# Kernel optimization log

Measured on AMD Instinct MI355X. Metric: run time of the kernel, lower is better.

The kernel has to match this reference:

```python
import jax, jax.numpy as jnp
import numpy as np

K_UNF = 11   # unfold kernel = 15 - 4
PAD = 1      # reflection padding for attention branch
KC = 5       # ConvBlock kernel_conv
HEADS = 4
CIN = 64
HD = CIN // HEADS  # head_dim = 16
EPS = 1e-5


def _unfold(x, k):
    # x: [b,C,H,W] -> [b, C*k*k, oh*ow] with torch.nn.Unfold ordering (c, kh, kw)
    b, C, H, W = x.shape
    oh, ow = H - k + 1, W - k + 1
    ih = jnp.arange(oh)[:, None] + jnp.arange(k)[None, :]  # [oh,k]
    iw = jnp.arange(ow)[:, None] + jnp.arange(k)[None, :]  # [ow,k]
    p = x[:, :, ih, :]          # [b,C,oh,k,W]
    p = p[:, :, :, :, iw]       # [b,C,oh,k,ow,k]
    p = p.transpose(0, 1, 3, 5, 2, 4)  # [b,C,kh,kw,oh,ow]
    return p.reshape(b, C * k * k, oh * ow)


def _bn_train(x):
    # BatchNorm2d in training mode, weight=1, bias=0 (fresh module defaults)
    m = x.mean(axis=(0, 2, 3), keepdims=True)
    v = x.var(axis=(0, 2, 3), keepdims=True)
    return (x - m) * jax.lax.rsqrt(v + EPS)


def setup_inputs() -> dict:
    key = jax.random.key(0)
    ks = jax.random.split(key, 6)
    b = 64
    s = 0.02
    x1 = jax.random.normal(ks[0], (b, CIN, 15, 15), jnp.float32)
    Wq = jax.random.normal(ks[1], (CIN, CIN), jnp.float32) * s
    Wk = jax.random.normal(ks[2], (CIN, CIN), jnp.float32) * s
    Wv = jax.random.normal(ks[3], (CIN, CIN), jnp.float32) * s
    fc_w = jax.random.normal(ks[4], (KC * KC, 3 * HEADS), jnp.float32) * s
    convg_w = jax.random.normal(ks[5], (CIN, CIN, 3, 3), jnp.float32) * s
    # dep_conv weight: deterministic one-hot shift kernels per reset_parameters
    dk = np.zeros((KC * KC, KC, KC), np.float32)
    for i in range(KC * KC):
        dk[i, i // KC, i % KC] = 1.0
    dep_w = jnp.asarray(np.broadcast_to(dk[None], (CIN, KC * KC, KC, KC)).copy())
    return {"x1": x1, "Wq": Wq, "Wk": Wk, "Wv": Wv, "fc_w": fc_w,
            "dep_w": dep_w, "convg_w": convg_w}


def reference(x1, Wq, Wk, Wv, fc_w, dep_w, convg_w):
    b, C, h, w = x1.shape  # h=w=15 (i=1 -> size=15)
    size = h
    # 1x1 qkv convs
    q = jnp.einsum('oc,bchw->bohw', Wq, x1)
    k = jnp.einsum('oc,bchw->bohw', Wk, x1)
    v = jnp.einsum('oc,bchw->bohw', Wv, x1)
    # ---- conv branch (ConvBlock) ----
    qkv = jnp.concatenate([t.reshape(b, HEADS, HD, h * w) for t in (q, k, v)], axis=1)  # [b,12,16,225]
    f_all = jnp.einsum('oc,bcds->bods', fc_w, qkv)                 # [b,25,16,225]
    f_conv = f_all.transpose(0, 2, 1, 3).reshape(b, HD * KC * KC, h, w)  # [b,400,15,15]
    out_conv = jax.lax.conv_general_dilated(
        f_conv, dep_w, (1, 1), 'VALID',
        dimension_numbers=('NCHW', 'OIHW', 'NCHW'),
        feature_group_count=HD)                                     # [b,64,11,11]; bias is None
    out_conv = _bn_train(out_conv)
    # ---- attention branch (UnfoldBlock + raw scaled QK^T, no softmax) ----
    def pad_unfold(t):
        tp = jnp.pad(t, ((0, 0), (0, 0), (PAD, PAD), (PAD, PAD)), mode='reflect')
        u = _unfold(tp, K_UNF).transpose(0, 2, 1)  # [b,49,7744]; pos_embed is zeros
        cls = jnp.zeros((b, 1, u.shape[-1]), u.dtype)  # cls token params are zeros
        return jnp.concatenate([cls, u], axis=1)       # [b,50,7744]
    uq, uk, uv = pad_unfold(q), pad_unfold(k), pad_unfold(v)
    N, Cq = uq.shape[1], uq.shape[2]
    query = uq.reshape(b, HEADS, N, Cq // HEADS)  # matches torch reshape semantics
    key_ = uk.reshape(b, HEADS, N, Cq // HEADS)
    val = uv.reshape(b, HEADS, N, Cq // HEADS)
    scaling = float(HD) ** -0.5
    att = jnp.einsum('bhnc,bhmc->bhnm', query, key_) * scaling   # [b,4,50,50]
    out_attn = jnp.einsum('bhnm,bhmc->bhnc', att, val)
    out_attn = out_attn.transpose(0, 2, 1, 3).reshape(b, N, Cq)
    out_attn = out_attn[:, 1, :].reshape(b, CIN, size - 4, size - 4)  # [b,64,11,11]
    out_attn = jax.lax.conv_general_dilated(
        out_attn, convg_w, (1, 1), ((1, 1), (1, 1)),
        dimension_numbers=('NCHW', 'OIHW', 'NCHW'))
    # rate1 and rate2 are filled with 0.5 every forward
    return out_conv * 0.5 + out_attn * 0.5
```

## Files before the change

kernel.cpp:

```cpp
#include <hip/hip_runtime.h>
#include <hip/hip_bf16.h>

#define B 64
#define CIN 64
#define HW 225
#define CQ 7744

__device__ __forceinline__ int reflect15(int t) {
    return t < 0 ? -t : (t > 14 ? 28 - t : t);
}
__device__ __forceinline__ int refp(int t) { return reflect15(t - 1); }

__global__ void qkv_kernel(const float* __restrict__ x1,
                           const float* __restrict__ Wq,
                           const float* __restrict__ Wk,
                           const float* __restrict__ Wv,
                           float* __restrict__ q, float* __restrict__ k, float* __restrict__ v) {
    int b = blockIdx.x;
    int t = blockIdx.y;
    const float* W = (t == 0) ? Wq : (t == 1) ? Wk : Wv;
    float* out = (t == 0) ? q : (t == 1) ? k : v;
    __shared__ float xs[CIN * HW];
    __shared__ float wsm[CIN * CIN];
    const float* xb = x1 + (size_t)b * CIN * HW;
    for (int i = threadIdx.x; i < CIN * HW; i += 512) xs[i] = xb[i];
    for (int i = threadIdx.x; i < CIN * CIN; i += 512) wsm[i] = W[i];
    __syncthreads();
    int og = threadIdx.x >> 5;
    int ls = threadIdx.x & 31;
    float a0[8] = {0,0,0,0,0,0,0,0};
    float a1[8] = {0,0,0,0,0,0,0,0};
    float a2[8] = {0,0,0,0,0,0,0,0};
    float a3[8] = {0,0,0,0,0,0,0,0};
    for (int c = 0; c < CIN; ++c) {
        const float* xc = xs + c * HW;
        float xv[8];
        #pragma unroll
        for (int j = 0; j < 8; ++j) {
            int s = ls + 32 * j;
            xv[j] = (s < HW) ? xc[s] : 0.f;
        }
        float w0 = wsm[(og)      * CIN + c];
        float w1 = wsm[(og + 16) * CIN + c];
        float w2 = wsm[(og + 32) * CIN + c];
        float w3 = wsm[(og + 48) * CIN + c];
        #pragma unroll
        for (int j = 0; j < 8; ++j) {
            a0[j] += w0 * xv[j];
            a1[j] += w1 * xv[j];
            a2[j] += w2 * xv[j];
            a3[j] += w3 * xv[j];
        }
    }
    float* ob = out + (size_t)b * CIN * HW;
    #pragma unroll
    for (int j = 0; j < 8; ++j) {
        int s = ls + 32 * j;
        if (s < HW) {
            ob[(og)      * HW + s] = a0[j];
            ob[(og + 16) * HW + s] = a1[j];
            ob[(og + 32) * HW + s] = a2[j];
            ob[(og + 48) * HW + s] = a3[j];
        }
    }
}

__global__ void conv5_kernel(const float* __restrict__ q, const float* __restrict__ k,
                             const float* __restrict__ v, const float* __restrict__ fc_w,
                             float* __restrict__ ocpre, float* __restrict__ stats) {
    int b = blockIdx.x, g = blockIdx.y;
    __shared__ float chs[12][HW];
    __shared__ float fw[300];
    __shared__ float red[128], red2[128];
    const float* srcs[3] = {q, k, v};
    for (int i = threadIdx.x; i < 12 * HW; i += blockDim.x) {
        int c = i / HW, s = i % HW;
        int t = c >> 2, hd = c & 3;
        chs[c][s] = srcs[t][(size_t)b * CIN * HW + (hd * 16 + g) * HW + s];
    }
    for (int i = threadIdx.x; i < 300; i += blockDim.x) fw[i] = fc_w[i];
    __syncthreads();
    float myval = 0.f;
    int yx = threadIdx.x;
    if (yx < 121) {
        int y = yx / 11, x = yx % 11;
        float acc = 0.f;
        #pragma unroll
        for (int c = 0; c < 12; ++c) {
            #pragma unroll
            for (int kh = 0; kh < 5; ++kh) {
                #pragma unroll
                for (int kw = 0; kw < 5; ++kw) {
                    acc += fw[(kh * 5 + kw) * 12 + c] * chs[c][(y + kh) * 15 + (x + kw)];
                }
            }
        }
        ocpre[((size_t)b * 16 + g) * 121 + yx] = acc;
        myval = acc;
    }
    red[threadIdx.x] = myval;
    red2[threadIdx.x] = myval * myval;
    __syncthreads();
    for (int s = 64; s > 0; s >>= 1) {
        if (threadIdx.x < s) {
            red[threadIdx.x] += red[threadIdx.x + s];
            red2[threadIdx.x] += red2[threadIdx.x + s];
        }
        __syncthreads();
    }
    if (threadIdx.x == 0) {
        atomicAdd(&stats[g], red[0]);
        atomicAdd(&stats[16 + g], red2[0]);
    }
}

__global__ void qk_kernel(const float* __restrict__ q, const float* __restrict__ k,
                          float* __restrict__ att_g) {
    int b = blockIdx.x, hh = blockIdx.y, qq = blockIdx.z;
    __shared__ float kp[16 * 289];
    __shared__ float qw[16 * 121];
    int tid = threadIdx.x;
    const float* kb = k + ((size_t)b * CIN + qq * 16) * HW;
    for (int i = tid; i < 16 * 289; i += 256) {
        int ch = i / 289, rr = i % 289;
        int yy = rr / 17, xx = rr % 17;
        kp[i] = kb[ch * HW + refp(yy) * 15 + refp(xx)];
    }
    {
        int gq = 50 * hh + 1;
        int rq = gq >> 2;
        if (rq == 0) {
            for (int i = tid; i < 16 * 121; i += 256) qw[i] = 0.f;
        } else {
            int cq = (gq & 3) * 16;
            int p = rq - 1, py0 = p / 7, px0 = p % 7;
            const float* qb = q + ((size_t)b * CIN + cq) * HW;
            for (int i = tid; i < 16 * 121; i += 256) {
                int cl = i / 121, rr = i % 121;
                int ki = rr / 11, kj = rr % 11;
                qw[i] = qb[cl * HW + refp(py0 + ki) * 15 + refp(px0 + kj)];
            }
        }
    }
    __syncthreads();
    int wave = tid >> 6, lane = tid & 63;
    int m0 = (qq - 2 * hh) & 3;
    int nt = (50 - m0 + 3) >> 2;
    float* ag = att_g + ((size_t)b * 4 + hh) * 64;
    for (int t = wave; t < nt; t += 4) {
        int m = m0 + t * 4;
        int g = 50 * hh + m;
        int r = g >> 2;
        float acc = 0.f;
        if (r > 0) {
            int p = r - 1, py = p / 7, px = p % 7;
            #pragma unroll
            for (int it = 0; it < 3; ++it) {
                int rw = lane + it * 64;
                if (rw < 176) {
                    int cl = rw / 11, ki = rw % 11;
                    const float* kr = kp + cl * 289 + (py + ki) * 17 + px;
                    const float* qr = qw + cl * 121 + ki * 11;
                    float s = 0.f;
                    #pragma unroll
                    for (int kj = 0; kj < 11; ++kj) s += qr[kj] * kr[kj];
                    acc += s;
                }
            }
            #pragma unroll
            for (int off = 32; off > 0; off >>= 1) acc += __shfl_xor(acc, off);
        }
        if (lane == 0) ag[m] = acc * 0.25f;
    }
}

__global__ void pv_kernel(const float* __restrict__ v, const float* __restrict__ att_g,
                          float* __restrict__ attn_img) {
    int b = blockIdx.x, hh = blockIdx.y, clg = blockIdx.z;
    __shared__ float vp[16 * 289];
    __shared__ float attmap[4 * 49];
    int tid = threadIdx.x;
    const float* vb = v + (size_t)b * CIN * HW;
    for (int i = tid; i < 16 * 289; i += 256) {
        int idx = i / 289, rr = i % 289;
        int qq2 = idx >> 2, cs = idx & 3;
        int yy = rr / 17, xx = rr % 17;
        vp[i] = vb[(qq2 * 16 + clg * 4 + cs) * HW + refp(yy) * 15 + refp(xx)];
    }
    if (tid < 4 * 49) attmap[tid] = 0.f;
    __syncthreads();
    if (tid < 50) {
        int g = 50 * hh + tid;
        int r = g >> 2;
        if (r > 0) attmap[(g & 3) * 49 + (r - 1)] = att_g[((size_t)b * 4 + hh) * 64 + tid];
    }
    __syncthreads();
    float* outp = attn_img + (size_t)b * CQ + hh * 1936 + clg * 4 * 121;
    if (tid < 242) {
        #pragma unroll
        for (int half = 0; half < 2; ++half) {
            int o = tid + half * 242;
            int cs = o / 121, yx = o % 121;
            int y = yx / 11, x = yx % 11;
            float acc = 0.f;
            #pragma unroll
            for (int qq2 = 0; qq2 < 4; ++qq2) {
                const float* vc = vp + (qq2 * 4 + cs) * 289 + y * 17 + x;
                const float* am = attmap + qq2 * 49;
                #pragma unroll
                for (int py = 0; py < 7; ++py) {
                    #pragma unroll
                    for (int px = 0; px < 7; ++px) {
                        acc += am[py * 7 + px] * vc[py * 17 + px];
                    }
                }
            }
            outp[cs * 121 + yx] = acc;
        }
    }
}

__global__ __launch_bounds__(512, 2) void final_kernel(
                             const float* __restrict__ ocpre, const float* __restrict__ stats,
                             const float* __restrict__ attn_img, const float* __restrict__ convg_w,
                             float* __restrict__ out) {
    int b = blockIdx.x, og = blockIdx.y;
    __shared__ float ap[CIN * 169];
    __shared__ float wsm[8 * CIN * 12];
    __shared__ float red[3 * 8 * 128];
    int tid = threadIdx.x;
    for (int i = tid; i < CIN * 169; i += 512) ap[i] = 0.f;
    for (int i = tid; i < 8 * CIN * 9; i += 512) {
        int oc = i / 9, t = i % 9;
        wsm[oc * 12 + t] = convg_w[(size_t)og * 8 * CIN * 9 + i];
    }
    __syncthreads();
    for (int i = tid; i < CIN * 121; i += 512) {
        int c = i / 121, ss = i % 121;
        ap[c * 169 + (ss / 11 + 1) * 13 + (ss % 11 + 1)] = attn_img[(size_t)b * CQ + i];
    }
    __syncthreads();
    int quarter = tid >> 7;
    int slot = tid & 127;
    int px = slot < 121 ? slot : 120;
    int y = px / 11, x = px % 11;
    float f0 = 0.f, f1 = 0.f, f2 = 0.f, f3 = 0.f, f4 = 0.f, f5 = 0.f, f6 = 0.f, f7 = 0.f;
    #pragma unroll 2
    for (int c16 = 0; c16 < 16; ++c16) {
        int c = quarter * 16 + c16;
        const float* apc = ap + c * 169 + y * 13 + x;
        float a00 = apc[0],  a01 = apc[1],  a02 = apc[2];
        float a10 = apc[13], a11 = apc[14], a12 = apc[15];
        float a20 = apc[26], a21 = apc[27], a22 = apc[28];
        const float4* wq = (const float4*)wsm;
        #pragma unroll
        for (int oo = 0; oo < 8; ++oo) {
            float4 wA = wq[(oo * 64 + c) * 3 + 0];
            float4 wB = wq[(oo * 64 + c) * 3 + 1];
            float4 wC = wq[(oo * 64 + c) * 3 + 2];
            float s = wA.x * a00 + wA.y * a01 + wA.z * a02
                    + wA.w * a10 + wB.x * a11 + wB.y * a12
                    + wB.z * a20 + wB.w * a21 + wC.x * a22;
            switch (oo) {
                case 0: f0 += s; break; case 1: f1 += s; break;
                case 2: f2 += s; break; case 3: f3 += s; break;
                case 4: f4 += s; break; case 5: f5 += s; break;
                case 6: f6 += s; break; case 7: f7 += s; break;
            }
        }
    }
    if (quarter > 0) {
        float* r = red + (quarter - 1) * 1024 + slot;
        r[0 * 128] = f0; r[1 * 128] = f1; r[2 * 128] = f2; r[3 * 128] = f3;
        r[4 * 128] = f4; r[5 * 128] = f5; r[6 * 128] = f6; r[7 * 128] = f7;
    }
    __syncthreads();
    if (quarter == 0 && slot < 121) {
        #pragma unroll
        for (int qq = 0; qq < 3; ++qq) {
            const float* r = red + qq * 1024 + slot;
            f0 += r[0 * 128]; f1 += r[1 * 128]; f2 += r[2 * 128]; f3 += r[3 * 128];
            f4 += r[4 * 128]; f5 += r[5 * 128]; f6 += r[6 * 128]; f7 += r[7 * 128];
        }
        int g0 = og * 2, g1 = og * 2 + 1;
        float m0 = stats[g0] * (1.f / 7744.f);
        float m1 = stats[g1] * (1.f / 7744.f);
        float v0 = stats[16 + g0] * (1.f / 7744.f) - m0 * m0;
        float v1 = stats[16 + g1] * (1.f / 7744.f) - m1 * m1;
        float r0 = rsqrtf(v0 + 1e-5f);
        float r1 = rsqrtf(v1 + 1e-5f);
        float bn0 = (ocpre[((size_t)b * 16 + g0) * 121 + slot] - m0) * r0;
        float bn1 = (ocpre[((size_t)b * 16 + g1) * 121 + slot] - m1) * r1;
        float* ob = out + ((size_t)b * CIN + og * 8) * 121 + slot;
        ob[0 * 121] = 0.5f * bn0 + 0.5f * f0;
        ob[1 * 121] = 0.5f * bn0 + 0.5f * f1;
        ob[2 * 121] = 0.5f * bn0 + 0.5f * f2;
        ob[3 * 121] = 0.5f * bn0 + 0.5f * f3;
        ob[4 * 121] = 0.5f * bn1 + 0.5f * f4;
        ob[5 * 121] = 0.5f * bn1 + 0.5f * f5;
        ob[6 * 121] = 0.5f * bn1 + 0.5f * f6;
        ob[7 * 121] = 0.5f * bn1 + 0.5f * f7;
    }
}

extern "C" void kernel_launch(void* const* d_in, const int* in_sizes, int n_in,
                              void* d_out, int out_size, void* d_ws, size_t ws_size,
                              hipStream_t stream) {
    const float* x1     = (const float*)d_in[0];
    const float* Wq     = (const float*)d_in[1];
    const float* Wk     = (const float*)d_in[2];
    const float* Wv     = (const float*)d_in[3];
    const float* fc_w   = (const float*)d_in[4];
    const float* convg_w = (const float*)d_in[6];
    float* out = (float*)d_out;

    char* ws = (char*)d_ws;
    float* q        = (float*)(ws);
    float* k        = (float*)(ws + 3686400);
    float* v        = (float*)(ws + 7372800);
    float* ocpre    = (float*)(ws + 11059200);
    float* stats    = (float*)(ws + 11554816);
    float* attn_img = (float*)(ws + 11555072);
    float* att_g    = (float*)(ws + 13537536);

    hipMemsetAsync(stats, 0, 32 * sizeof(float), stream);
    hipLaunchKernelGGL(qkv_kernel, dim3(64, 3), dim3(512), 0, stream, x1, Wq, Wk, Wv, q, k, v);
    hipLaunchKernelGGL(conv5_kernel, dim3(64, 16), dim3(128), 0, stream, q, k, v, fc_w, ocpre, stats);
    hipLaunchKernelGGL(qk_kernel, dim3(64, 4, 4), dim3(256), 0, stream, q, k, att_g);
    hipLaunchKernelGGL(pv_kernel, dim3(64, 4, 4), dim3(256), 0, stream, v, att_g, attn_img);
    hipLaunchKernelGGL(final_kernel, dim3(64, 8), dim3(512), 0, stream, ocpre, stats, attn_img, convg_w, out);
}
```

Measured before the change: 167.6 us.

## Register-tile qkv, restructure pv, fold memset, read weights directly from global

The qkv kernel now uses 256 threads, each computing an 8x8 register tile from padded shared x and a transposed weight copy with float4 loads. It also zeroes the stats buffer itself, which removes the separate memset. pv_kernel merges the channel-group grid dimension so one block loads all 64 padded v channels, and it broadcasts attention weights with readlane while each thread computes six output pixels. conv5 and final now read fc_w and convg_w straight from global memory instead of staging them in shared memory. The stats zeroing depends on kernel ordering on the same stream, and the direct global weight reads may cost more if they are not turned into scalar loads.

```diff
diff --git a/kernel.cpp b/kernel.cpp
--- a/kernel.cpp
+++ b/kernel.cpp
@@ -5,62 +5,62 @@
 #define CIN 64
 #define HW 225
 #define CQ 7744
+#define XSP 232
 
 __device__ __forceinline__ int reflect15(int t) {
     return t < 0 ? -t : (t > 14 ? 28 - t : t);
 }
 __device__ __forceinline__ int refp(int t) { return reflect15(t - 1); }
 
-__global__ void qkv_kernel(const float* __restrict__ x1,
+__global__ __launch_bounds__(256) void qkv_kernel(const float* __restrict__ x1,
                            const float* __restrict__ Wq,
                            const float* __restrict__ Wk,
                            const float* __restrict__ Wv,
-                           float* __restrict__ q, float* __restrict__ k, float* __restrict__ v) {
+                           float* __restrict__ q, float* __restrict__ k, float* __restrict__ v,
+                           float* __restrict__ stats) {
     int b = blockIdx.x;
     int t = blockIdx.y;
+    if (b == 0 && t == 0 && threadIdx.x < 32) stats[threadIdx.x] = 0.f;
     const float* W = (t == 0) ? Wq : (t == 1) ? Wk : Wv;
     float* out = (t == 0) ? q : (t == 1) ? k : v;
-    __shared__ float xs[CIN * HW];
-    __shared__ float wsm[CIN * CIN];
+    __shared__ float xs[CIN * XSP];
+    __shared__ float wsmT[CIN * CIN];
     const float* xb = x1 + (size_t)b * CIN * HW;
-    for (int i = threadIdx.x; i < CIN * HW; i += 512) xs[i] = xb[i];
-    for (int i = threadIdx.x; i < CIN * CIN; i += 512) wsm[i] = W[i];
+    for (int i = threadIdx.x; i < CIN * XSP; i += 256) {
+        int c = i / XSP, s = i % XSP;
+        xs[i] = (s < HW) ? xb[c * HW + s] : 0.f;
+    }
+    for (int i = threadIdx.x; i < CIN * CIN; i += 256) {
+        wsmT[i] = W[(i & 63) * CIN + (i >> 6)];
+    }
     __syncthreads();
     int og = threadIdx.x >> 5;
     int ls = threadIdx.x & 31;
-    float a0[8] = {0,0,0,0,0,0,0,0};
-    float a1[8] = {0,0,0,0,0,0,0,0};
-    float a2[8] = {0,0,0,0,0,0,0,0};
-    float a3[8] = {0,0,0,0,0,0,0,0};
+    float acc[8][8];
+    #pragma unroll
+    for (int m = 0; m < 8; ++m)
+        #pragma unroll
+        for (int j = 0; j < 8; ++j) acc[m][j] = 0.f;
     for (int c = 0; c < CIN; ++c) {
-        const float* xc = xs + c * HW;
-        float xv[8];
-        #pragma unroll
-        for (int j = 0; j < 8; ++j) {
-            int s = ls + 32 * j;
-            xv[j] = (s < HW) ? xc[s] : 0.f;
-        }
-        float w0 = wsm[(og)      * CIN + c];
-        float w1 = wsm[(og + 16) * CIN + c];
-        float w2 = wsm[(og + 32) * CIN + c];
-        float w3 = wsm[(og + 48) * CIN + c];
-        #pragma unroll
-        for (int j = 0; j < 8; ++j) {
-            a0[j] += w0 * xv[j];
-            a1[j] += w1 * xv[j];
-            a2[j] += w2 * xv[j];
-            a3[j] += w3 * xv[j];
-        }
+        float4 xv0 = *(const float4*)(xs + c * XSP + ls * 8);
+        float4 xv1 = *(const float4*)(xs + c * XSP + ls * 8 + 4);
+        float4 wv0 = *(const float4*)(wsmT + c * CIN + og * 8);
+        float4 wv1 = *(const float4*)(wsmT + c * CIN + og * 8 + 4);
+        float xr[8] = {xv0.x, xv0.y, xv0.z, xv0.w, xv1.x, xv1.y, xv1.z, xv1.w};
+        float wr[8] = {wv0.x, wv0.y, wv0.z, wv0.w, wv1.x, wv1.y, wv1.z, wv1.w};
+        #pragma unroll
+        for (int m = 0; m < 8; ++m)
+            #pragma unroll
+            for (int j = 0; j < 8; ++j) acc[m][j] += wr[m] * xr[j];
     }
     float* ob = out + (size_t)b * CIN * HW;
     #pragma unroll
-    for (int j = 0; j < 8; ++j) {
-        int s = ls + 32 * j;
-        if (s < HW) {
-            ob[(og)      * HW + s] = a0[j];
-            ob[(og + 16) * HW + s] = a1[j];
-            ob[(og + 32) * HW + s] = a2[j];
-            ob[(og + 48) * HW + s] = a3[j];
+    for (int m = 0; m < 8; ++m) {
+        int o = og * 8 + m;
+        #pragma unroll
+        for (int j = 0; j < 8; ++j) {
+            int px = ls * 8 + j;
+            if (px < HW) ob[o * HW + px] = acc[m][j];
         }
     }
 }
@@ -70,7 +70,6 @@
                              float* __restrict__ ocpre, float* __restrict__ stats) {
     int b = blockIdx.x, g = blockIdx.y;
     __shared__ float chs[12][HW];
-    __shared__ float fw[300];
     __shared__ float red[128], red2[128];
     const float* srcs[3] = {q, k, v};
     for (int i = threadIdx.x; i < 12 * HW; i += blockDim.x) {
@@ -78,7 +77,6 @@
         int t = c >> 2, hd = c & 3;
         chs[c][s] = srcs[t][(size_t)b * CIN * HW + (hd * 16 + g) * HW + s];
     }
-    for (int i = threadIdx.x; i < 300; i += blockDim.x) fw[i] = fc_w[i];
     __syncthreads();
     float myval = 0.f;
     int yx = threadIdx.x;
@@ -91,7 +89,7 @@
             for (int kh = 0; kh < 5; ++kh) {
                 #pragma unroll
                 for (int kw = 0; kw < 5; ++kw) {
-                    acc += fw[(kh * 5 + kw) * 12 + c] * chs[c][(y + kh) * 15 + (x + kw)];
+                    acc += fc_w[(kh * 5 + kw) * 12 + c] * chs[c][(y + kh) * 15 + (x + kw)];
                 }
             }
         }
@@ -174,49 +172,60 @@
     }
 }
 
-__global__ void pv_kernel(const float* __restrict__ v, const float* __restrict__ att_g,
+__global__ __launch_bounds__(512) void pv_kernel(const float* __restrict__ v,
+                          const float* __restrict__ att_g,
                           float* __restrict__ attn_img) {
-    int b = blockIdx.x, hh = blockIdx.y, clg = blockIdx.z;
-    __shared__ float vp[16 * 289];
-    __shared__ float attmap[4 * 49];
+    int b = blockIdx.x, hh = blockIdx.y;
+    __shared__ float vp[64 * 289 + 16];
+    __shared__ float am[4 * 49];
     int tid = threadIdx.x;
     const float* vb = v + (size_t)b * CIN * HW;
-    for (int i = tid; i < 16 * 289; i += 256) {
-        int idx = i / 289, rr = i % 289;
-        int qq2 = idx >> 2, cs = idx & 3;
+    for (int i = tid; i < 64 * 289; i += 512) {
+        int ch = i / 289, rr = i % 289;
         int yy = rr / 17, xx = rr % 17;
-        vp[i] = vb[(qq2 * 16 + clg * 4 + cs) * HW + refp(yy) * 15 + refp(xx)];
-    }
-    if (tid < 4 * 49) attmap[tid] = 0.f;
+        vp[i] = vb[ch * HW + refp(yy) * 15 + refp(xx)];
+    }
+    if (tid < 196) am[tid] = 0.f;
     __syncthreads();
     if (tid < 50) {
         int g = 50 * hh + tid;
         int r = g >> 2;
-        if (r > 0) attmap[(g & 3) * 49 + (r - 1)] = att_g[((size_t)b * 4 + hh) * 64 + tid];
-    }
-    __syncthreads();
-    float* outp = attn_img + (size_t)b * CQ + hh * 1936 + clg * 4 * 121;
-    if (tid < 242) {
-        #pragma unroll
-        for (int half = 0; half < 2; ++half) {
-            int o = tid + half * 242;
-            int cs = o / 121, yx = o % 121;
-            int y = yx / 11, x = yx % 11;
-            float acc = 0.f;
-            #pragma unroll
-            for (int qq2 = 0; qq2 < 4; ++qq2) {
-                const float* vc = vp + (qq2 * 4 + cs) * 289 + y * 17 + x;
-                const float* am = attmap + qq2 * 49;
+        if (r > 0) am[(g & 3) * 49 + (r - 1)] = att_g[((size_t)b * 4 + hh) * 64 + tid];
+    }
+    __syncthreads();
+    int lane = tid & 63;
+    int w = tid;
+    int cl = w / 22, rem = w % 22;
+    int y = rem >> 1, xh = rem & 1;
+    int x0 = xh * 6;
+    int nx = xh ? 5 : 6;
+    bool act = w < 352;
+    float acc[6] = {0, 0, 0, 0, 0, 0};
+    #pragma unroll
+    for (int qq = 0; qq < 4; ++qq) {
+        float amv = 0.f;
+        if (lane < 49) amv = am[qq * 49 + lane];
+        if (act) {
+            const float* base = vp + (qq * 16 + cl) * 289;
+            #pragma unroll
+            for (int py = 0; py < 7; ++py) {
+                const float* row = base + (y + py) * 17 + x0;
+                float rv[12];
                 #pragma unroll
-                for (int py = 0; py < 7; ++py) {
+                for (int j = 0; j < 12; ++j) rv[j] = row[j];
+                #pragma unroll
+                for (int px = 0; px < 7; ++px) {
+                    float a = __uint_as_float(
+                        __builtin_amdgcn_readlane(__float_as_uint(amv), py * 7 + px));
                     #pragma unroll
-                    for (int px = 0; px < 7; ++px) {
-                        acc += am[py * 7 + px] * vc[py * 17 + px];
-                    }
+                    for (int i = 0; i < 6; ++i) acc[i] += a * rv[px + i];
                 }
             }
-            outp[cs * 121 + yx] = acc;
-        }
+        }
+    }
+    if (act) {
+        float* outp = attn_img + (size_t)b * CQ + hh * 1936 + cl * 121 + y * 11 + x0;
+        for (int i = 0; i < nx; ++i) outp[i] = acc[i];
     }
 }
 
@@ -226,41 +235,32 @@
                              float* __restrict__ out) {
     int b = blockIdx.x, og = blockIdx.y;
     __shared__ float ap[CIN * 169];
-    __shared__ float wsm[8 * CIN * 12];
     __shared__ float red[3 * 8 * 128];
     int tid = threadIdx.x;
     for (int i = tid; i < CIN * 169; i += 512) ap[i] = 0.f;
-    for (int i = tid; i < 8 * CIN * 9; i += 512) {
-        int oc = i / 9, t = i % 9;
-        wsm[oc * 12 + t] = convg_w[(size_t)og * 8 * CIN * 9 + i];
-    }
     __syncthreads();
     for (int i = tid; i < CIN * 121; i += 512) {
         int c = i / 121, ss = i % 121;
         ap[c * 169 + (ss / 11 + 1) * 13 + (ss % 11 + 1)] = attn_img[(size_t)b * CQ + i];
     }
     __syncthreads();
-    int quarter = tid >> 7;
+    int qu = __builtin_amdgcn_readfirstlane(tid >> 7);
     int slot = tid & 127;
     int px = slot < 121 ? slot : 120;
     int y = px / 11, x = px % 11;
     float f0 = 0.f, f1 = 0.f, f2 = 0.f, f3 = 0.f, f4 = 0.f, f5 = 0.f, f6 = 0.f, f7 = 0.f;
-    #pragma unroll 2
+    const float* wb = convg_w + ((size_t)og * 8 * CIN + qu * 16) * 9;
     for (int c16 = 0; c16 < 16; ++c16) {
-        int c = quarter * 16 + c16;
-        const float* apc = ap + c * 169 + y * 13 + x;
+        const float* apc = ap + (qu * 16 + c16) * 169 + y * 13 + x;
         float a00 = apc[0],  a01 = apc[1],  a02 = apc[2];
         float a10 = apc[13], a11 = apc[14], a12 = apc[15];
         float a20 = apc[26], a21 = apc[27], a22 = apc[28];
-        const float4* wq = (const float4*)wsm;
         #pragma unroll
         for (int oo = 0; oo < 8; ++oo) {
-            float4 wA = wq[(oo * 64 + c) * 3 + 0];
-            float4 wB = wq[(oo * 64 + c) * 3 + 1];
-            float4 wC = wq[(oo * 64 + c) * 3 + 2];
-            float s = wA.x * a00 + wA.y * a01 + wA.z * a02
-                    + wA.w * a10 + wB.x * a11 + wB.y * a12
-                    + wB.z * a20 + wB.w * a21 + wC.x * a22;
+            const float* w = wb + (oo * CIN + c16) * 9;
+            float s = w[0] * a00 + w[1] * a01 + w[2] * a02
+                    + w[3] * a10 + w[4] * a11 + w[5] * a12
+                    + w[6] * a20 + w[7] * a21 + w[8] * a22;
             switch (oo) {
                 case 0: f0 += s; break; case 1: f1 += s; break;
                 case 2: f2 += s; break; case 3: f3 += s; break;
@@ -269,13 +269,13 @@
             }
         }
     }
-    if (quarter > 0) {
-        float* r = red + (quarter - 1) * 1024 + slot;
+    if (qu > 0) {
+        float* r = red + (qu - 1) * 1024 + slot;
         r[0 * 128] = f0; r[1 * 128] = f1; r[2 * 128] = f2; r[3 * 128] = f3;
         r[4 * 128] = f4; r[5 * 128] = f5; r[6 * 128] = f6; r[7 * 128] = f7;
     }
     __syncthreads();
-    if (quarter == 0 && slot < 121) {
+    if (qu == 0 && slot < 121) {
         #pragma unroll
         for (int qq = 0; qq < 3; ++qq) {
             const float* r = red + qq * 1024 + slot;
@@ -323,10 +323,9 @@
     float* attn_img = (float*)(ws + 11555072);
     float* att_g    = (float*)(ws + 13537536);
 
-    hipMemsetAsync(stats, 0, 32 * sizeof(float), stream);
-    hipLaunchKernelGGL(qkv_kernel, dim3(64, 3), dim3(512), 0, stream, x1, Wq, Wk, Wv, q, k, v);
+    hipLaunchKernelGGL(qkv_kernel, dim3(64, 3), dim3(256), 0, stream, x1, Wq, Wk, Wv, q, k, v, stats);
     hipLaunchKernelGGL(conv5_kernel, dim3(64, 16), dim3(128), 0, stream, q, k, v, fc_w, ocpre, stats);
     hipLaunchKernelGGL(qk_kernel, dim3(64, 4, 4), dim3(256), 0, stream, q, k, att_g);
-    hipLaunchKernelGGL(pv_kernel, dim3(64, 4, 4), dim3(256), 0, stream, v, att_g, attn_img);
+    hipLaunchKernelGGL(pv_kernel, dim3(64, 4), dim3(512), 0, stream, v, att_g, attn_img);
     hipLaunchKernelGGL(final_kernel, dim3(64, 8), dim3(512), 0, stream, ocpre, stats, attn_img, convg_w, out);
 }
```

New measurement: 178.6 us. 1.07x slower.
